# Kernel tuning notes

Measured on AMD Instinct MI355X. Metric: run time of the kernel, lower is better.

## Reference

```python
import jax, jax.numpy as jnp
import numpy as np
import math

HEAD_SIZE = 64
WHERE_CONST = -10000.0


def setup_inputs() -> dict:
    key = jax.random.key(0)
    k1, k2, k3 = jax.random.split(key, 3)
    shape = (4, 16, 2048, 64)  # [B, H, S, D]
    q = jax.random.normal(k1, shape, dtype=jnp.float32)
    k = jax.random.normal(k2, shape, dtype=jnp.float32)
    v = jax.random.normal(k3, shape, dtype=jnp.float32)
    return {"q": q, "k": k, "v": v}


def reference(q, k, v):
    # scores: [B, H, Sq, Sk]
    scale = 1.0 / math.sqrt(HEAD_SIZE)
    scores = jnp.einsum('bhqd,bhkd->bhqk', q, k) * scale
    q_len, k_len = q.shape[-2], k.shape[-2]
    causal_mask = jnp.tril(jnp.ones((q_len, k_len), dtype=bool))[None, None]
    scores = jnp.where(causal_mask, scores, WHERE_CONST)
    probs = jax.nn.softmax(scores, axis=-1)
    # dropout rate is 0.0 -> identity
    out = jnp.einsum('bhqk,bhkd->bhqd', probs, v)  # [B, H, S, D]
    out = jnp.swapaxes(out, 1, 2)                  # [B, S, H, D]
    B, S, H, D = out.shape
    return out.reshape(B, S, H * D)
```

## Files before the change

### kernel.cpp

```cpp
#include <hip/hip_runtime.h>
#include <hip/hip_bf16.h>

typedef __bf16 bf16x8_t __attribute__((ext_vector_type(8)));
typedef float  f32x4_t  __attribute__((ext_vector_type(4)));
typedef short  short8_t __attribute__((ext_vector_type(8)));
typedef short  short4_t __attribute__((ext_vector_type(4)));

#define NB   4
#define NH   16
#define SEQ  2048
#define HD   64
#define QT   64
#define BKV  64
#define NQT  (SEQ / QT)
#define LSTR 72

#define MASK2 (-14426.950408889634f)
#define QSCL  (0.18033688011112042f)

__device__ __forceinline__ int swz(int rowi, int blk) {
    return rowi * LSTR + (((blk) ^ (rowi >> 3)) & 7) * 8;
}

__global__ void __launch_bounds__(256)
fa_fwd(const float* __restrict__ qg,
       const float* __restrict__ kg,
       const float* __restrict__ vg,
       float* __restrict__ outg) {
    __shared__ alignas(16) short k_lds[BKV * LSTR];
    __shared__ alignas(16) short vt_lds[HD * LSTR];
    __shared__ alignas(16) short p_lds[QT * LSTR];

    const int tid  = threadIdx.x;
    const int wave = tid >> 6;
    const int lane = tid & 63;
    const int l16  = lane & 15;
    const int quad = lane >> 4;

    const int bh = blockIdx.x;
    const int z  = blockIdx.y;

    const size_t base = (size_t)bh * SEQ * HD;
    const float* qp = qg + base;
    const float* kp = kg + base;
    const float* vp = vg + base;

    const int sr = tid >> 4;
    const int cb = tid & 15;
    const int d0 = cb * 4;

    f32x4_t kreg[4], vreg[4];

    auto issue = [&](int kt0) {
        const float* kr = kp + (size_t)(kt0 + 4 * sr) * HD + d0;
        const float* vr = vp + (size_t)(kt0 + 4 * sr) * HD + d0;
        #pragma unroll
        for (int i = 0; i < 4; ++i) {
            kreg[i] = *(const f32x4_t*)(kr + i * HD);
            vreg[i] = *(const f32x4_t*)(vr + i * HD);
        }
    };

    auto stage = [&]() {
        #pragma unroll
        for (int i = 0; i < 4; ++i) {
            const int r0 = 4 * sr + i;
            short4_t kw;
            #pragma unroll
            for (int j = 0; j < 4; ++j) kw[j] = __builtin_bit_cast(short, (__bf16)kreg[i][j]);
            *(short4_t*)&k_lds[swz(r0, cb >> 1) + (cb & 1) * 4] = kw;
        }
        #pragma unroll
        for (int j = 0; j < 4; ++j) {
            short4_t vw;
            #pragma unroll
            for (int i = 0; i < 4; ++i) vw[i] = __builtin_bit_cast(short, (__bf16)vreg[i][j]);
            *(short4_t*)&vt_lds[swz(d0 + j, sr >> 1) + (sr & 1) * 4] = vw;
        }
    };

    const int qloc = wave * 16 + l16;
    const int b = bh >> 4;
    const int h = bh & 15;
    const f32x4_t zero4 = {0.0f, 0.0f, 0.0f, 0.0f};

    issue(0);

    #pragma unroll 1
    for (int run = 0; run < 2; ++run) {
        const int qt = (run == 0) ? (NQT - 1 - z) : z;
        const int q0 = qt * QT;
        const int nt = qt + 1;

        bf16x8_t qf0, qf1;
        {
            const float* qr = qp + (size_t)(q0 + wave * 16 + l16) * HD;
            f32x4_t a0 = *(const f32x4_t*)(qr + quad * 8);
            f32x4_t a1 = *(const f32x4_t*)(qr + quad * 8 + 4);
            f32x4_t a2 = *(const f32x4_t*)(qr + 32 + quad * 8);
            f32x4_t a3 = *(const f32x4_t*)(qr + 32 + quad * 8 + 4);
            #pragma unroll
            for (int j = 0; j < 4; ++j) {
                qf0[j]     = (__bf16)(a0[j] * QSCL);
                qf0[4 + j] = (__bf16)(a1[j] * QSCL);
                qf1[j]     = (__bf16)(a2[j] * QSCL);
                qf1[4 + j] = (__bf16)(a3[j] * QSCL);
            }
        }

        f32x4_t o_acc[4];
        #pragma unroll
        for (int c = 0; c < 4; ++c) o_acc[c] = zero4;
        float m_x = MASK2, l_x = 0.0f;

        #pragma unroll 1
        for (int t = 0; t < nt; ++t) {
            const int kt0 = t * BKV;
            __syncthreads();
            stage();
            __syncthreads();
            if (t + 1 < nt) issue(kt0 + BKV);
            else if (run == 0) issue(0);

            f32x4_t s_acc[4];
            #pragma unroll
            for (int c = 0; c < 4; ++c) s_acc[c] = zero4;
            __builtin_amdgcn_s_setprio(1);
            #pragma unroll
            for (int c = 0; c < 4; ++c) {
                const int kvrow = c * 16 + l16;
                bf16x8_t kf0 = __builtin_bit_cast(bf16x8_t, *(const short8_t*)&k_lds[swz(kvrow, quad)]);
                bf16x8_t kf1 = __builtin_bit_cast(bf16x8_t, *(const short8_t*)&k_lds[swz(kvrow, quad + 4)]);
                s_acc[c] = __builtin_amdgcn_mfma_f32_16x16x32_bf16(kf0, qf0, s_acc[c], 0, 0, 0);
                s_acc[c] = __builtin_amdgcn_mfma_f32_16x16x32_bf16(kf1, qf1, s_acc[c], 0, 0, 0);
            }
            __builtin_amdgcn_s_setprio(0);

            float sv[4][4];
            float vmax = MASK2;
            const bool diag = (t == nt - 1);
            #pragma unroll
            for (int c = 0; c < 4; ++c) {
                #pragma unroll
                for (int r = 0; r < 4; ++r) {
                    float x = s_acc[c][r];
                    if (diag && (c * 16 + quad * 4 + r > qloc)) x = MASK2;
                    sv[c][r] = x;
                    vmax = fmaxf(vmax, x);
                }
            }
            vmax = fmaxf(vmax, __shfl_xor(vmax, 16));
            vmax = fmaxf(vmax, __shfl_xor(vmax, 32));

            if (__any((int)(vmax > m_x))) {
                float mn = fmaxf(m_x, vmax);
                float a  = __builtin_amdgcn_exp2f(m_x - mn);
                m_x = mn;
                l_x *= a;
                float ar[4];
                #pragma unroll
                for (int r = 0; r < 4; ++r)
                    ar[r] = __shfl(a, (lane & 48) | (quad * 4 + r));
                #pragma unroll
                for (int c = 0; c < 4; ++c)
                    #pragma unroll
                    for (int r = 0; r < 4; ++r)
                        o_acc[c][r] *= ar[r];
            }

            const int prow = wave * 16 + l16;
            float rs = 0.0f;
            #pragma unroll
            for (int c = 0; c < 4; ++c) {
                short4_t pw;
                #pragma unroll
                for (int r = 0; r < 4; ++r) {
                    float p = __builtin_amdgcn_exp2f(sv[c][r] - m_x);
                    rs += p;
                    pw[r] = __builtin_bit_cast(short, (__bf16)p);
                }
                *(short4_t*)&p_lds[swz(prow, 2 * c + (quad >> 1)) + (quad & 1) * 4] = pw;
            }
            rs += __shfl_xor(rs, 16);
            rs += __shfl_xor(rs, 32);
            l_x += rs;


            bf16x8_t pf0 = __builtin_bit_cast(bf16x8_t, *(const short8_t*)&p_lds[swz(prow, quad)]);
            bf16x8_t pf1 = __builtin_bit_cast(bf16x8_t, *(const short8_t*)&p_lds[swz(prow, quad + 4)]);
            __builtin_amdgcn_s_setprio(1);
            #pragma unroll
            for (int c = 0; c < 4; ++c) {
                const int d = c * 16 + l16;
                bf16x8_t b0 = __builtin_bit_cast(bf16x8_t, *(const short8_t*)&vt_lds[swz(d, quad)]);
                bf16x8_t b1 = __builtin_bit_cast(bf16x8_t, *(const short8_t*)&vt_lds[swz(d, quad + 4)]);
                o_acc[c] = __builtin_amdgcn_mfma_f32_16x16x32_bf16(pf0, b0, o_acc[c], 0, 0, 0);
                o_acc[c] = __builtin_amdgcn_mfma_f32_16x16x32_bf16(pf1, b1, o_acc[c], 0, 0, 0);
            }
            __builtin_amdgcn_s_setprio(0);
        }

        #pragma unroll
        for (int r = 0; r < 4; ++r) {
            const float lr = __shfl(l_x, (lane & 48) | (quad * 4 + r));
            const float inv_l = 1.0f / fmaxf(lr, 1e-30f);
            const int row = q0 + wave * 16 + quad * 4 + r;
            float* op = outg + ((size_t)b * SEQ + row) * (NH * HD) + h * HD;
            #pragma unroll
            for (int c = 0; c < 4; ++c) {
                float val = o_acc[c][r] * inv_l;
                unsigned bits = __builtin_bit_cast(unsigned, val);
                if ((bits & 0x7F800000u) == 0x7F800000u) val = 0.0f;
                op[c * 16 + l16] = val;
            }
        }
    }
}

extern "C" void kernel_launch(void* const* d_in, const int* in_sizes, int n_in,
                              void* d_out, int out_size, void* d_ws, size_t ws_size,
                              hipStream_t stream) {
    const float* q = (const float*)d_in[0];
    const float* k = (const float*)d_in[1];
    const float* v = (const float*)d_in[2];
    float* out = (float*)d_out;
    dim3 grid(NB * NH, NQT / 2);
    fa_fwd<<<grid, 256, 0, stream>>>(q, k, v, out);
}
```

Baseline: 207.7 us.

## Pre-convert K/V to swizzled bf16 tiles and stream via async global-to-LDS loads

A new prep kernel converts K and V to bf16 in workspace, using a pre-swizzled layout with V already transposed. The attention kernel then copies each tile straight into double-buffered LDS with global_load_lds, so per-iteration conversion and register staging disappear and one barrier is dropped. The grid also changes from paired q-tiles per block to one q-tile per block, processed heaviest first. This costs an extra kernel launch and a workspace round trip, and it falls back to a register-staged kernel when the workspace is too small.

```diff
diff --git a/kernel.cpp b/kernel.cpp
--- a/kernel.cpp
+++ b/kernel.cpp
@@ -5,31 +5,71 @@
 typedef float  f32x4_t  __attribute__((ext_vector_type(4)));
 typedef short  short8_t __attribute__((ext_vector_type(8)));
 typedef short  short4_t __attribute__((ext_vector_type(4)));
+typedef unsigned short ushort4_t __attribute__((ext_vector_type(4)));
+
+typedef const __attribute__((address_space(1))) unsigned int* gptr_t;
+typedef __attribute__((address_space(3))) unsigned int* lptr_t;
 
 #define NB   4
 #define NH   16
 #define SEQ  2048
 #define HD   64
-#define QT   64
+#define BQ   64
 #define BKV  64
-#define NQT  (SEQ / QT)
-#define LSTR 72
+#define NT   (SEQ / BKV)
+#define TILE_SH (BKV * HD)
 
 #define MASK2 (-14426.950408889634f)
 #define QSCL  (0.18033688011112042f)
 
-__device__ __forceinline__ int swz(int rowi, int blk) {
-    return rowi * LSTR + (((blk) ^ (rowi >> 3)) & 7) * 8;
+__device__ __forceinline__ int xaddr(int row, int blk) {
+    return row * 64 + (((blk ^ row) & 7) << 3);
+}
+
+__global__ void __launch_bounds__(256)
+prep_kv(const float* __restrict__ kg, const float* __restrict__ vg,
+        unsigned short* __restrict__ kimg, unsigned short* __restrict__ vimg) {
+    const int t   = blockIdx.x;
+    const int bh  = blockIdx.y;
+    const int tid = threadIdx.x;
+    const int sr  = tid >> 4;
+    const int cb  = tid & 15;
+    const int d0  = cb * 4;
+
+    const size_t gbase = ((size_t)bh * SEQ + (size_t)t * BKV) * HD;
+    const size_t ibase = ((size_t)bh * NT + t) * TILE_SH;
+
+    f32x4_t v4[4];
+    #pragma unroll
+    for (int i = 0; i < 4; ++i) {
+        const int r = 4 * sr + i;
+        f32x4_t k4 = *(const f32x4_t*)(kg + gbase + (size_t)r * HD + d0);
+        v4[i]      = *(const f32x4_t*)(vg + gbase + (size_t)r * HD + d0);
+        ushort4_t kw;
+        #pragma unroll
+        for (int j = 0; j < 4; ++j) kw[j] = __builtin_bit_cast(unsigned short, (__bf16)k4[j]);
+        *(ushort4_t*)&kimg[ibase + xaddr(r, cb >> 1) + (cb & 1) * 4] = kw;
+    }
+    #pragma unroll
+    for (int j = 0; j < 4; ++j) {
+        ushort4_t vw;
+        #pragma unroll
+        for (int i = 0; i < 4; ++i) vw[i] = __builtin_bit_cast(unsigned short, (__bf16)v4[i][j]);
+        *(ushort4_t*)&vimg[ibase + xaddr(d0 + j, sr >> 1) + (sr & 1) * 4] = vw;
+    }
+}
+
+__device__ __forceinline__ void gl16(const unsigned short* g, short* l) {
+    __builtin_amdgcn_global_load_lds((gptr_t)g, (lptr_t)l, 16, 0, 0);
 }
 
 __global__ void __launch_bounds__(256)
 fa_fwd(const float* __restrict__ qg,
-       const float* __restrict__ kg,
-       const float* __restrict__ vg,
+       const unsigned short* __restrict__ kimg,
+       const unsigned short* __restrict__ vimg,
        float* __restrict__ outg) {
-    __shared__ alignas(16) short k_lds[BKV * LSTR];
-    __shared__ alignas(16) short vt_lds[HD * LSTR];
-    __shared__ alignas(16) short p_lds[QT * LSTR];
+    __shared__ alignas(16) short kv_lds[2][2][TILE_SH];
+    __shared__ alignas(16) short p_lds[64 * 64];
 
     const int tid  = threadIdx.x;
     const int wave = tid >> 6;
@@ -38,17 +78,213 @@
     const int quad = lane >> 4;
 
     const int bh = blockIdx.x;
-    const int z  = blockIdx.y;
+    const int qt = (int)gridDim.y - 1 - (int)blockIdx.y;
+    const int q0 = qt * BQ;
+
+    const float* qp = qg + (size_t)bh * SEQ * HD;
+    const unsigned short* kb = kimg + (size_t)bh * NT * TILE_SH;
+    const unsigned short* vb = vimg + (size_t)bh * NT * TILE_SH;
+
+    bf16x8_t qf0, qf1;
+    {
+        const float* qr = qp + (size_t)(q0 + wave * 16 + l16) * HD;
+        f32x4_t a0 = *(const f32x4_t*)(qr + quad * 8);
+        f32x4_t a1 = *(const f32x4_t*)(qr + quad * 8 + 4);
+        f32x4_t a2 = *(const f32x4_t*)(qr + 32 + quad * 8);
+        f32x4_t a3 = *(const f32x4_t*)(qr + 32 + quad * 8 + 4);
+        #pragma unroll
+        for (int j = 0; j < 4; ++j) {
+            qf0[j]     = (__bf16)(a0[j] * QSCL);
+            qf0[4 + j] = (__bf16)(a1[j] * QSCL);
+            qf1[j]     = (__bf16)(a2[j] * QSCL);
+            qf1[4 + j] = (__bf16)(a3[j] * QSCL);
+        }
+    }
+
+    f32x4_t o_acc[4];
+    const f32x4_t zero4 = {0.0f, 0.0f, 0.0f, 0.0f};
+    #pragma unroll
+    for (int c = 0; c < 4; ++c) o_acc[c] = zero4;
+    float m_x = MASK2, l_x = 0.0f;
+
+    auto stage = [&](int buf, int t) {
+        const unsigned short* kg_ = kb + (size_t)t * TILE_SH;
+        const unsigned short* vg_ = vb + (size_t)t * TILE_SH;
+        #pragma unroll
+        for (int r = 0; r < 2; ++r) {
+            const int loff = r * 2048 + wave * 512;
+            const int goff = loff + lane * 8;
+            gl16(kg_ + goff, &kv_lds[buf][0][loff]);
+            gl16(vg_ + goff, &kv_lds[buf][1][loff]);
+        }
+    };
+
+    const int qloc = wave * 16 + l16;
+    const int nt = qt + 1;
+    int cur = 0;
+
+    stage(0, 0);
+
+    #pragma unroll 1
+    for (int t = 0; t < nt; ++t) {
+        __syncthreads();
+        if (t + 1 < nt) stage(cur ^ 1, t + 1);
+
+        const short* kt_ = kv_lds[cur][0];
+        const short* vt_ = kv_lds[cur][1];
+
+        f32x4_t s_acc[4];
+        #pragma unroll
+        for (int c = 0; c < 4; ++c) s_acc[c] = zero4;
+        __builtin_amdgcn_s_setprio(1);
+        #pragma unroll
+        for (int c = 0; c < 4; ++c) {
+            const int kvrow = c * 16 + l16;
+            bf16x8_t kf0 = __builtin_bit_cast(bf16x8_t, *(const short8_t*)&kt_[xaddr(kvrow, quad)]);
+            bf16x8_t kf1 = __builtin_bit_cast(bf16x8_t, *(const short8_t*)&kt_[xaddr(kvrow, quad + 4)]);
+            s_acc[c] = __builtin_amdgcn_mfma_f32_16x16x32_bf16(kf0, qf0, s_acc[c], 0, 0, 0);
+            s_acc[c] = __builtin_amdgcn_mfma_f32_16x16x32_bf16(kf1, qf1, s_acc[c], 0, 0, 0);
+        }
+        __builtin_amdgcn_s_setprio(0);
+
+        float sv[4][4];
+        float vmax = MASK2;
+        const bool diag = (t == nt - 1);
+        #pragma unroll
+        for (int c = 0; c < 4; ++c) {
+            #pragma unroll
+            for (int r = 0; r < 4; ++r) {
+                float x = s_acc[c][r];
+                if (diag && (c * 16 + quad * 4 + r > qloc)) x = MASK2;
+                sv[c][r] = x;
+                vmax = fmaxf(vmax, x);
+            }
+        }
+        vmax = fmaxf(vmax, __shfl_xor(vmax, 16));
+        vmax = fmaxf(vmax, __shfl_xor(vmax, 32));
+
+        if (__any((int)(vmax > m_x))) {
+            float mn = fmaxf(m_x, vmax);
+            float a  = __builtin_amdgcn_exp2f(m_x - mn);
+            m_x = mn;
+            l_x *= a;
+            float ar[4];
+            #pragma unroll
+            for (int r = 0; r < 4; ++r)
+                ar[r] = __shfl(a, (lane & 48) | (quad * 4 + r));
+            #pragma unroll
+            for (int c = 0; c < 4; ++c)
+                #pragma unroll
+                for (int r = 0; r < 4; ++r)
+                    o_acc[c][r] *= ar[r];
+        }
+
+        const int prow = wave * 16 + l16;
+        float rs = 0.0f;
+        #pragma unroll
+        for (int c = 0; c < 4; ++c) {
+            short4_t pw;
+            #pragma unroll
+            for (int r = 0; r < 4; ++r) {
+                float p = __builtin_amdgcn_exp2f(sv[c][r] - m_x);
+                rs += p;
+                pw[r] = __builtin_bit_cast(short, (__bf16)p);
+            }
+            *(short4_t*)&p_lds[xaddr(prow, 2 * c + (quad >> 1)) + (quad & 1) * 4] = pw;
+        }
+        rs += __shfl_xor(rs, 16);
+        rs += __shfl_xor(rs, 32);
+        l_x += rs;
+
+
+        bf16x8_t pf0 = __builtin_bit_cast(bf16x8_t, *(const short8_t*)&p_lds[xaddr(prow, quad)]);
+        bf16x8_t pf1 = __builtin_bit_cast(bf16x8_t, *(const short8_t*)&p_lds[xaddr(prow, quad + 4)]);
+        __builtin_amdgcn_s_setprio(1);
+        #pragma unroll
+        for (int c = 0; c < 4; ++c) {
+            const int d = c * 16 + l16;
+            bf16x8_t b0 = __builtin_bit_cast(bf16x8_t, *(const short8_t*)&vt_[xaddr(d, quad)]);
+            bf16x8_t b1 = __builtin_bit_cast(bf16x8_t, *(const short8_t*)&vt_[xaddr(d, quad + 4)]);
+            o_acc[c] = __builtin_amdgcn_mfma_f32_16x16x32_bf16(pf0, b0, o_acc[c], 0, 0, 0);
+            o_acc[c] = __builtin_amdgcn_mfma_f32_16x16x32_bf16(pf1, b1, o_acc[c], 0, 0, 0);
+        }
+        __builtin_amdgcn_s_setprio(0);
+
+        cur ^= 1;
+    }
+
+    const int b = bh >> 4;
+    const int h = bh & 15;
+    #pragma unroll
+    for (int r = 0; r < 4; ++r) {
+        const float lr = __shfl(l_x, (lane & 48) | (quad * 4 + r));
+        const float inv_l = 1.0f / fmaxf(lr, 1e-30f);
+        const int row = q0 + wave * 16 + quad * 4 + r;
+        float* op = outg + ((size_t)b * SEQ + row) * (NH * HD) + h * HD;
+        #pragma unroll
+        for (int c = 0; c < 4; ++c) {
+            float val = o_acc[c][r] * inv_l;
+            unsigned bits = __builtin_bit_cast(unsigned, val);
+            if ((bits & 0x7F800000u) == 0x7F800000u) val = 0.0f;
+            op[c * 16 + l16] = val;
+        }
+    }
+}
+
+#define LSTR 72
+__device__ __forceinline__ int swz(int rowi, int blk) {
+    return rowi * LSTR + (((blk) ^ (rowi >> 3)) & 7) * 8;
+}
+
+__global__ void __launch_bounds__(256)
+fa_fwd_fb(const float* __restrict__ qg,
+          const float* __restrict__ kg,
+          const float* __restrict__ vg,
+          float* __restrict__ outg) {
+    __shared__ alignas(16) short k_lds[BKV * LSTR];
+    __shared__ alignas(16) short vt_lds[HD * LSTR];
+    __shared__ alignas(16) short p_lds2[BQ * LSTR];
+
+    const int tid  = threadIdx.x;
+    const int wave = tid >> 6;
+    const int lane = tid & 63;
+    const int l16  = lane & 15;
+    const int quad = lane >> 4;
+
+    const int bh = blockIdx.x;
+    const int qt = (int)gridDim.y - 1 - (int)blockIdx.y;
+    const int q0 = qt * BQ;
 
     const size_t base = (size_t)bh * SEQ * HD;
     const float* qp = qg + base;
     const float* kp = kg + base;
     const float* vp = vg + base;
 
+    bf16x8_t qf0, qf1;
+    {
+        const float* qr = qp + (size_t)(q0 + wave * 16 + l16) * HD;
+        f32x4_t a0 = *(const f32x4_t*)(qr + quad * 8);
+        f32x4_t a1 = *(const f32x4_t*)(qr + quad * 8 + 4);
+        f32x4_t a2 = *(const f32x4_t*)(qr + 32 + quad * 8);
+        f32x4_t a3 = *(const f32x4_t*)(qr + 32 + quad * 8 + 4);
+        #pragma unroll
+        for (int j = 0; j < 4; ++j) {
+            qf0[j]     = (__bf16)(a0[j] * QSCL);
+            qf0[4 + j] = (__bf16)(a1[j] * QSCL);
+            qf1[j]     = (__bf16)(a2[j] * QSCL);
+            qf1[4 + j] = (__bf16)(a3[j] * QSCL);
+        }
+    }
+
+    f32x4_t o_acc[4];
+    const f32x4_t zero4 = {0.0f, 0.0f, 0.0f, 0.0f};
+    #pragma unroll
+    for (int c = 0; c < 4; ++c) o_acc[c] = zero4;
+    float m_x = MASK2, l_x = 0.0f;
+
     const int sr = tid >> 4;
     const int cb = tid & 15;
     const int d0 = cb * 4;
-
     f32x4_t kreg[4], vreg[4];
 
     auto issue = [&](int kt0) {
@@ -60,8 +296,7 @@
             vreg[i] = *(const f32x4_t*)(vr + i * HD);
         }
     };
-
-    auto stage = [&]() {
+    auto stg = [&]() {
         #pragma unroll
         for (int i = 0; i < 4; ++i) {
             const int r0 = 4 * sr + i;
@@ -79,140 +314,98 @@
         }
     };
 
+    issue(0);
     const int qloc = wave * 16 + l16;
+    const int nt = qt + 1;
+    for (int t = 0; t < nt; ++t) {
+        __syncthreads();
+        stg();
+        __syncthreads();
+        if (t + 1 < nt) issue((t + 1) * BKV);
+
+        f32x4_t s_acc[4];
+        #pragma unroll
+        for (int c = 0; c < 4; ++c) s_acc[c] = zero4;
+        #pragma unroll
+        for (int c = 0; c < 4; ++c) {
+            const int kvrow = c * 16 + l16;
+            bf16x8_t kf0 = __builtin_bit_cast(bf16x8_t, *(const short8_t*)&k_lds[swz(kvrow, quad)]);
+            bf16x8_t kf1 = __builtin_bit_cast(bf16x8_t, *(const short8_t*)&k_lds[swz(kvrow, quad + 4)]);
+            s_acc[c] = __builtin_amdgcn_mfma_f32_16x16x32_bf16(kf0, qf0, s_acc[c], 0, 0, 0);
+            s_acc[c] = __builtin_amdgcn_mfma_f32_16x16x32_bf16(kf1, qf1, s_acc[c], 0, 0, 0);
+        }
+
+        float sv[4][4];
+        float vmax = MASK2;
+        const bool diag = (t == nt - 1);
+        #pragma unroll
+        for (int c = 0; c < 4; ++c)
+            #pragma unroll
+            for (int r = 0; r < 4; ++r) {
+                float x = s_acc[c][r];
+                if (diag && (c * 16 + quad * 4 + r > qloc)) x = MASK2;
+                sv[c][r] = x;
+                vmax = fmaxf(vmax, x);
+            }
+        vmax = fmaxf(vmax, __shfl_xor(vmax, 16));
+        vmax = fmaxf(vmax, __shfl_xor(vmax, 32));
+        if (__any((int)(vmax > m_x))) {
+            float mn = fmaxf(m_x, vmax);
+            float a  = __builtin_amdgcn_exp2f(m_x - mn);
+            m_x = mn;
+            l_x *= a;
+            float ar[4];
+            #pragma unroll
+            for (int r = 0; r < 4; ++r) ar[r] = __shfl(a, (lane & 48) | (quad * 4 + r));
+            #pragma unroll
+            for (int c = 0; c < 4; ++c)
+                #pragma unroll
+                for (int r = 0; r < 4; ++r) o_acc[c][r] *= ar[r];
+        }
+
+        const int prow = wave * 16 + l16;
+        float rs = 0.0f;
+        #pragma unroll
+        for (int c = 0; c < 4; ++c) {
+            short4_t pw;
+            #pragma unroll
+            for (int r = 0; r < 4; ++r) {
+                float p = __builtin_amdgcn_exp2f(sv[c][r] - m_x);
+                rs += p;
+                pw[r] = __builtin_bit_cast(short, (__bf16)p);
+            }
+            *(short4_t*)&p_lds2[swz(prow, 2 * c + (quad >> 1)) + (quad & 1) * 4] = pw;
+        }
+        rs += __shfl_xor(rs, 16);
+        rs += __shfl_xor(rs, 32);
+        l_x += rs;
+
+        bf16x8_t pf0 = __builtin_bit_cast(bf16x8_t, *(const short8_t*)&p_lds2[swz(prow, quad)]);
+        bf16x8_t pf1 = __builtin_bit_cast(bf16x8_t, *(const short8_t*)&p_lds2[swz(prow, quad + 4)]);
+        #pragma unroll
+        for (int c = 0; c < 4; ++c) {
+            const int d = c * 16 + l16;
+            bf16x8_t b0 = __builtin_bit_cast(bf16x8_t, *(const short8_t*)&vt_lds[swz(d, quad)]);
+            bf16x8_t b1 = __builtin_bit_cast(bf16x8_t, *(const short8_t*)&vt_lds[swz(d, quad + 4)]);
+            o_acc[c] = __builtin_amdgcn_mfma_f32_16x16x32_bf16(pf0, b0, o_acc[c], 0, 0, 0);
+            o_acc[c] = __builtin_amdgcn_mfma_f32_16x16x32_bf16(pf1, b1, o_acc[c], 0, 0, 0);
+        }
+    }
+
     const int b = bh >> 4;
     const int h = bh & 15;
-    const f32x4_t zero4 = {0.0f, 0.0f, 0.0f, 0.0f};
-
-    issue(0);
-
-    #pragma unroll 1
-    for (int run = 0; run < 2; ++run) {
-        const int qt = (run == 0) ? (NQT - 1 - z) : z;
-        const int q0 = qt * QT;
-        const int nt = qt + 1;
-
-        bf16x8_t qf0, qf1;
-        {
-            const float* qr = qp + (size_t)(q0 + wave * 16 + l16) * HD;
-            f32x4_t a0 = *(const f32x4_t*)(qr + quad * 8);
-            f32x4_t a1 = *(const f32x4_t*)(qr + quad * 8 + 4);
-            f32x4_t a2 = *(const f32x4_t*)(qr + 32 + quad * 8);
-            f32x4_t a3 = *(const f32x4_t*)(qr + 32 + quad * 8 + 4);
-            #pragma unroll
-            for (int j = 0; j < 4; ++j) {
-                qf0[j]     = (__bf16)(a0[j] * QSCL);
-                qf0[4 + j] = (__bf16)(a1[j] * QSCL);
-                qf1[j]     = (__bf16)(a2[j] * QSCL);
-                qf1[4 + j] = (__bf16)(a3[j] * QSCL);
-            }
-        }
-
-        f32x4_t o_acc[4];
-        #pragma unroll
-        for (int c = 0; c < 4; ++c) o_acc[c] = zero4;
-        float m_x = MASK2, l_x = 0.0f;
-
-        #pragma unroll 1
-        for (int t = 0; t < nt; ++t) {
-            const int kt0 = t * BKV;
-            __syncthreads();
-            stage();
-            __syncthreads();
-            if (t + 1 < nt) issue(kt0 + BKV);
-            else if (run == 0) issue(0);
-
-            f32x4_t s_acc[4];
-            #pragma unroll
-            for (int c = 0; c < 4; ++c) s_acc[c] = zero4;
-            __builtin_amdgcn_s_setprio(1);
-            #pragma unroll
-            for (int c = 0; c < 4; ++c) {
-                const int kvrow = c * 16 + l16;
-                bf16x8_t kf0 = __builtin_bit_cast(bf16x8_t, *(const short8_t*)&k_lds[swz(kvrow, quad)]);
-                bf16x8_t kf1 = __builtin_bit_cast(bf16x8_t, *(const short8_t*)&k_lds[swz(kvrow, quad + 4)]);
-                s_acc[c] = __builtin_amdgcn_mfma_f32_16x16x32_bf16(kf0, qf0, s_acc[c], 0, 0, 0);
-                s_acc[c] = __builtin_amdgcn_mfma_f32_16x16x32_bf16(kf1, qf1, s_acc[c], 0, 0, 0);
-            }
-            __builtin_amdgcn_s_setprio(0);
-
-            float sv[4][4];
-            float vmax = MASK2;
-            const bool diag = (t == nt - 1);
-            #pragma unroll
-            for (int c = 0; c < 4; ++c) {
-                #pragma unroll
-                for (int r = 0; r < 4; ++r) {
-                    float x = s_acc[c][r];
-                    if (diag && (c * 16 + quad * 4 + r > qloc)) x = MASK2;
-                    sv[c][r] = x;
-                    vmax = fmaxf(vmax, x);
-                }
-            }
-            vmax = fmaxf(vmax, __shfl_xor(vmax, 16));
-            vmax = fmaxf(vmax, __shfl_xor(vmax, 32));
-
-            if (__any((int)(vmax > m_x))) {
-                float mn = fmaxf(m_x, vmax);
-                float a  = __builtin_amdgcn_exp2f(m_x - mn);
-                m_x = mn;
-                l_x *= a;
-                float ar[4];
-                #pragma unroll
-                for (int r = 0; r < 4; ++r)
-                    ar[r] = __shfl(a, (lane & 48) | (quad * 4 + r));
-                #pragma unroll
-                for (int c = 0; c < 4; ++c)
-                    #pragma unroll
-                    for (int r = 0; r < 4; ++r)
-                        o_acc[c][r] *= ar[r];
-            }
-
-            const int prow = wave * 16 + l16;
-            float rs = 0.0f;
-            #pragma unroll
-            for (int c = 0; c < 4; ++c) {
-                short4_t pw;
-                #pragma unroll
-                for (int r = 0; r < 4; ++r) {
-                    float p = __builtin_amdgcn_exp2f(sv[c][r] - m_x);
-                    rs += p;
-                    pw[r] = __builtin_bit_cast(short, (__bf16)p);
-                }
-                *(short4_t*)&p_lds[swz(prow, 2 * c + (quad >> 1)) + (quad & 1) * 4] = pw;
-            }
-            rs += __shfl_xor(rs, 16);
-            rs += __shfl_xor(rs, 32);
-            l_x += rs;
-
-
-            bf16x8_t pf0 = __builtin_bit_cast(bf16x8_t, *(const short8_t*)&p_lds[swz(prow, quad)]);
-            bf16x8_t pf1 = __builtin_bit_cast(bf16x8_t, *(const short8_t*)&p_lds[swz(prow, quad + 4)]);
-            __builtin_amdgcn_s_setprio(1);
-            #pragma unroll
-            for (int c = 0; c < 4; ++c) {
-                const int d = c * 16 + l16;
-                bf16x8_t b0 = __builtin_bit_cast(bf16x8_t, *(const short8_t*)&vt_lds[swz(d, quad)]);
-                bf16x8_t b1 = __builtin_bit_cast(bf16x8_t, *(const short8_t*)&vt_lds[swz(d, quad + 4)]);
-                o_acc[c] = __builtin_amdgcn_mfma_f32_16x16x32_bf16(pf0, b0, o_acc[c], 0, 0, 0);
-                o_acc[c] = __builtin_amdgcn_mfma_f32_16x16x32_bf16(pf1, b1, o_acc[c], 0, 0, 0);
-            }
-            __builtin_amdgcn_s_setprio(0);
-        }
-
-        #pragma unroll
-        for (int r = 0; r < 4; ++r) {
-            const float lr = __shfl(l_x, (lane & 48) | (quad * 4 + r));
-            const float inv_l = 1.0f / fmaxf(lr, 1e-30f);
-            const int row = q0 + wave * 16 + quad * 4 + r;
-            float* op = outg + ((size_t)b * SEQ + row) * (NH * HD) + h * HD;
-            #pragma unroll
-            for (int c = 0; c < 4; ++c) {
-                float val = o_acc[c][r] * inv_l;
-                unsigned bits = __builtin_bit_cast(unsigned, val);
-                if ((bits & 0x7F800000u) == 0x7F800000u) val = 0.0f;
-                op[c * 16 + l16] = val;
-            }
+    #pragma unroll
+    for (int r = 0; r < 4; ++r) {
+        const float lr = __shfl(l_x, (lane & 48) | (quad * 4 + r));
+        const float inv_l = 1.0f / fmaxf(lr, 1e-30f);
+        const int row = q0 + wave * 16 + quad * 4 + r;
+        float* op = outg + ((size_t)b * SEQ + row) * (NH * HD) + h * HD;
+        #pragma unroll
+        for (int c = 0; c < 4; ++c) {
+            float val = o_acc[c][r] * inv_l;
+            unsigned bits = __builtin_bit_cast(unsigned, val);
+            if ((bits & 0x7F800000u) == 0x7F800000u) val = 0.0f;
+            op[c * 16 + l16] = val;
         }
     }
 }
@@ -224,6 +417,16 @@
     const float* k = (const float*)d_in[1];
     const float* v = (const float*)d_in[2];
     float* out = (float*)d_out;
-    dim3 grid(NB * NH, NQT / 2);
-    fa_fwd<<<grid, 256, 0, stream>>>(q, k, v, out);
-}
+
+    const size_t img_sh = (size_t)NB * NH * NT * TILE_SH;
+    const size_t need   = 2 * img_sh * sizeof(unsigned short);
+
+    if (d_ws != nullptr && ws_size >= need) {
+        unsigned short* kimg = (unsigned short*)d_ws;
+        unsigned short* vimg = kimg + img_sh;
+        prep_kv<<<dim3(NT, NB * NH), 256, 0, stream>>>(k, v, kimg, vimg);
+        fa_fwd<<<dim3(NB * NH, SEQ / BQ), 256, 0, stream>>>(q, kimg, vimg, out);
+    } else {
+        fa_fwd_fb<<<dim3(NB * NH, SEQ / BQ), 256, 0, stream>>>(q, k, v, out);
+    }
+}
```

Result: faster. 201.2 us (-3.1%).
